# Kernel optimization log

Hardware: AMD Instinct MI355X
Metric: run time of the kernel (lower is better)

The kernel has to match this reference:

```python
import jax, jax.numpy as jnp
import numpy as np

N_NODES = 100000
N_EDGES = 1600000
HIDDEN_DIM = 64
EIGS_DIM = 32


def setup_inputs() -> dict:
    key = jax.random.key(0)
    k1, k2, k3, k4, k5 = jax.random.split(key, 5)
    q = jax.random.normal(k1, (N_NODES, HIDDEN_DIM), dtype=jnp.float32)
    k = jax.random.normal(k2, (N_NODES, HIDDEN_DIM), dtype=jnp.float32)
    v = jax.random.normal(k3, (N_NODES, HIDDEN_DIM), dtype=jnp.float32)
    eigs = jax.random.normal(k4, (N_NODES, EIGS_DIM), dtype=jnp.float32)
    lambda0 = jnp.zeros((1,), dtype=jnp.float32)  # nn.Parameter(torch.zeros(1))
    indices = jax.random.randint(k5, (2, N_EDGES), 0, N_NODES, dtype=jnp.int64)
    return {"q": q, "k": k, "v": v, "eigs": eigs, "lambda0": lambda0,
            "indices": indices}


def reference(q, k, v, eigs, lambda0, indices):
    n = q.shape[0]
    inv_sqrt_dim = 1.0 / jnp.sqrt(jnp.asarray(q.shape[1], dtype=q.dtype))
    i0 = indices[0]  # destination/row node per edge
    i1 = indices[1]  # source/col node per edge

    # per-edge attention logits: gather-dot-product
    x = jnp.sum(q[i0] * k[i1], axis=-1) * inv_sqrt_dim          # [E]
    y = jnp.sum(eigs[i0] * eigs[i1], axis=-1)                   # [E]
    s = x + jnp.exp(lambda0[0]) * y                             # [E]

    # sparse softmax: clamp(exp(s), -5, 5) then segment-normalize by row sum
    e = jnp.clip(jnp.exp(s), -5.0, 5.0)                         # [E]
    denom = jax.ops.segment_sum(e, i0, num_segments=n)          # [N]
    denom = jnp.where(denom == 0.0, 1.0, denom)
    w = e / denom[i0]                                           # [E]

    # spmm: out[r] = sum_{edges with row r} w_e * v[col_e]
    out = jax.ops.segment_sum(w[:, None] * v[i1], i0, num_segments=n)  # [N, D]
    return out
```

## Files before the change

### kernel.cpp

```cpp
#include <hip/hip_runtime.h>
#include <hip/hip_fp16.h>


#define HD 64
#define ED 32
#define CAP 64
#define RPP 256
#define PSHIFT 8
#define D1 15
#define SLICE 16
#define NBIN 512
#define SPILL_CAP 65536

struct h4 { __half2 a, b; };

__global__ void p1_wide_kernel(const int* __restrict__ idx, int n_edges,
                               int NP, int chunk, long long pcap,
                               int* __restrict__ part,
                               long long* __restrict__ spill,
                               int* __restrict__ spill_cnt,
                               int* __restrict__ flag,
                               const float* __restrict__ kf,
                               const float* __restrict__ vf,
                               const float* __restrict__ ef,
                               __half* __restrict__ k16,
                               __half* __restrict__ v16,
                               __half* __restrict__ e16,
                               long long nk4, long long ne4) {
    extern __shared__ int sm[];
    int tid = threadIdx.x;

    if (blockIdx.x >= NBIN) {
        if (k16 == nullptr) return;
        long long gt = (long long)(blockIdx.x - NBIN) * 256 + tid;
        long long gs = (long long)(gridDim.x - NBIN) * 256;
        for (long long t = gt; t < nk4; t += gs) {
            float4 f = ((const float4*)kf)[t];
            h4 h;
            h.a = __floats2half2_rn(f.x, f.y);
            h.b = __floats2half2_rn(f.z, f.w);
            ((h4*)k16)[t] = h;
        }
        for (long long t = gt; t < nk4; t += gs) {
            float4 f = ((const float4*)vf)[t];
            h4 h;
            h.a = __floats2half2_rn(f.x, f.y);
            h.b = __floats2half2_rn(f.z, f.w);
            ((h4*)v16)[t] = h;
        }
        for (long long t = gt; t < ne4; t += gs) {
            float4 f = ((const float4*)ef)[t];
            h4 h;
            h.a = __floats2half2_rn(f.x, f.y);
            h.b = __floats2half2_rn(f.z, f.w);
            ((h4*)e16)[t] = h;
        }
        return;
    }

    int* cnt  = sm;
    int* bins = sm + NP;

    for (int i = tid; i < NP; i += 256) cnt[i] = 0;
    __syncthreads();

    int e0 = blockIdx.x * chunk;
    int n  = n_edges - e0; if (n > chunk) n = chunk; if (n < 0) n = 0;

    for (int i = tid; i < n; i += 256) {
        int e = e0 + i;
        int r = idx[e];
        int c = idx[n_edges + e];
        int p = r >> PSHIFT;
        int w = ((r & (RPP - 1)) << 17) | c;
        int pos = atomicAdd(&cnt[p], 1);
        if (pos < D1) {
            bins[p * D1 + pos] = w;
        } else {
            int s = atomicAdd(spill_cnt, 1);
            if (s < SPILL_CAP) spill[s] = ((long long)r << 32) | (unsigned)c;
            else *flag = 1;
        }
    }
    __syncthreads();

    int g16 = tid >> 4;
    int sl  = tid & 15;
    for (int p = g16; p < NP; p += 16) {
        int m = cnt[p]; if (m > D1) m = D1;
        long long base = (long long)p * pcap + (long long)blockIdx.x * SLICE;
        int val = (sl == 0) ? m
                : (sl <= m) ? bins[p * D1 + sl - 1] : 0;
        part[base + sl] = val;
    }
}

__global__ void p2_bucket_kernel(const int* __restrict__ part,
                                 const long long* __restrict__ spill,
                                 const int* __restrict__ spill_cnt,
                                 const int* __restrict__ flag,
                                 const int* __restrict__ idx, int n_edges,
                                 int* __restrict__ count,
                                 int* __restrict__ bucket, int n_nodes,
                                 long long pcap) {
    __shared__ int cnt2[RPP / 2];
    __shared__ int win[(RPP / 2) * CAP];
    int tid = threadIdx.x;
    if (tid < RPP / 2) cnt2[tid] = 0;
    __syncthreads();

    int p    = blockIdx.x >> 1;
    int half = blockIdx.x & 1;

    if (*flag == 0) {
        int g  = tid >> 4;
        int sl = tid & 15;
        const int* prow = part + (long long)p * pcap;
        for (int b = g; b < NBIN; b += 16) {
            int val = prow[b * SLICE + sl];
            int m = __shfl(val, 0, 16);
            if (m > D1) m = D1;
            if (sl >= 1 && sl <= m) {
                int rl = val >> 17;
                if ((rl >> 7) == half) {
                    int rh = rl & 127;
                    int c  = val & 0x1FFFF;
                    int pos = atomicAdd(&cnt2[rh], 1);
                    if (pos < CAP) win[(rh << 6) + pos] = c;
                }
            }
        }
        int ns = *spill_cnt; if (ns > SPILL_CAP) ns = SPILL_CAP;
        for (int i = tid; i < ns; i += 256) {
            long long wc = spill[i];
            int r = (int)(wc >> 32);
            if ((r >> PSHIFT) == p && (((r >> 7) & 1) == half)) {
                int rh = r & 127;
                int c  = (int)(wc & 0xFFFFFFFFLL);
                int pos = atomicAdd(&cnt2[rh], 1);
                if (pos < CAP) win[(rh << 6) + pos] = c;
            }
        }
    } else {
        for (int i = tid; i < n_edges; i += 256) {
            int r = idx[i];
            if ((r >> PSHIFT) == p && (((r >> 7) & 1) == half)) {
                int rh = r & 127;
                int c  = idx[n_edges + i];
                int pos = atomicAdd(&cnt2[rh], 1);
                if (pos < CAP) win[(rh << 6) + pos] = c;
            }
        }
    }
    __syncthreads();

    int r0 = (p << PSHIFT) + (half << 7);
    int rows = n_nodes - r0;
    if (rows > RPP / 2) rows = RPP / 2;
    if (rows > 0) {
        int nint4 = rows * (CAP / 4);
        int4* dst = (int4*)(bucket + (long long)r0 * CAP);
        const int4* src = (const int4*)win;
        for (int i = tid; i < nint4; i += 256) dst[i] = src[i];
        if (tid < rows) count[r0 + tid] = cnt2[tid];
    }
}

__global__ void bucket_scatter_kernel(const int* __restrict__ idx,
                                      int* __restrict__ count,
                                      int* __restrict__ bucket, int n_edges) {
    int t = blockIdx.x * blockDim.x + threadIdx.x;
    if (t < n_edges) {
        int r = idx[t];
        int c = idx[n_edges + t];
        int p = atomicAdd(&count[r], 1);
        if (p < CAP) bucket[(long long)r * CAP + p] = c;
    }
}

__global__ void row16_kernel(const float* __restrict__ q,
                             const __half* __restrict__ k16,
                             const __half* __restrict__ v16,
                             const float* __restrict__ eigs,
                             const __half* __restrict__ e16,
                             const float* __restrict__ lambda0,
                             const int* __restrict__ counts,
                             const int* __restrict__ col,
                             const float* __restrict__ kf,
                             const float* __restrict__ vf,
                             const int* __restrict__ idx, int n_edges,
                             float* __restrict__ out, int n_nodes) {
    long long tid = (long long)blockIdx.x * blockDim.x + threadIdx.x;
    int r = (int)(tid >> 6);
    if (r >= n_nodes) return;
    int lane = threadIdx.x & 63;
    int sub = lane & 15;
    int grp = lane >> 4;

    int deg = counts[r];
    const float expL = __expf(lambda0[0]);

    if (deg > CAP) {
        float qs = q[(long long)r * HD + lane] * 0.125f;
        float gs = (lane < ED) ? eigs[(long long)r * ED + lane] * expL : 0.f;
        float accs = 0.f, den = 0.f;
        for (int base = 0; base < n_edges; base += 64) {
            int e = base + lane;
            int rr = (e < n_edges) ? idx[e] : -1;
            int cc = (e < n_edges) ? idx[n_edges + e] : 0;
            unsigned long long mm = __ballot(rr == r);
            while (mm) {
                int b = __ffsll(mm) - 1;
                mm &= mm - 1;
                int c = __shfl(cc, b, 64);
                float kb = kf[(long long)c * HD + lane];
                float gb = (lane < ED) ? eigs[(long long)c * ED + lane] : 0.f;
                float s = qs * kb + gs * gb;
                #pragma unroll
                for (int off = 32; off > 0; off >>= 1) s += __shfl_xor(s, off, 64);
                float e1 = fminf(__expf(s), 5.0f);
                den += e1;
                accs += e1 * vf[(long long)c * HD + lane];
            }
        }
        float inv = (den == 0.f) ? 1.f : __frcp_rn(den);
        out[(long long)r * HD + lane] = accs * inv;
        return;
    }

    long long start = (long long)r * CAP;

    float4 qa = *(const float4*)(q    + (long long)r * HD + sub * 4);
    float2 ga = *(const float2*)(eigs + (long long)r * ED + sub * 2);
    qa.x *= 0.125f; qa.y *= 0.125f; qa.z *= 0.125f; qa.w *= 0.125f;
    ga.x *= expL;   ga.y *= expL;

    float4 acc = make_float4(0.f, 0.f, 0.f, 0.f);
    float den = 0.f;

    for (int base = 0; base < deg; base += 64) {
        int m = deg - base; if (m > 64) m = 64;
        int cl = (lane < m) ? col[start + base + lane] : 0;
        for (int j = 0; j < m; j += 16) {
            int c1 = __shfl(cl, j + grp,      64);
            int c2 = __shfl(cl, j + 4 + grp,  64);
            int c3 = __shfl(cl, j + 8 + grp,  64);
            int c4 = __shfl(cl, j + 12 + grp, 64);
            h4 kb1 = *(const h4*)(k16 + (long long)c1 * HD + sub * 4);
            __half2 gh1 = *(const __half2*)(e16 + (long long)c1 * ED + sub * 2);
            h4 vv1 = *(const h4*)(v16 + (long long)c1 * HD + sub * 4);
            h4 kb2 = *(const h4*)(k16 + (long long)c2 * HD + sub * 4);
            __half2 gh2 = *(const __half2*)(e16 + (long long)c2 * ED + sub * 2);
            h4 vv2 = *(const h4*)(v16 + (long long)c2 * HD + sub * 4);
            h4 kb3 = *(const h4*)(k16 + (long long)c3 * HD + sub * 4);
            __half2 gh3 = *(const __half2*)(e16 + (long long)c3 * ED + sub * 2);
            h4 vv3 = *(const h4*)(v16 + (long long)c3 * HD + sub * 4);
            h4 kb4 = *(const h4*)(k16 + (long long)c4 * HD + sub * 4);
            __half2 gh4 = *(const __half2*)(e16 + (long long)c4 * ED + sub * 2);
            h4 vv4 = *(const h4*)(v16 + (long long)c4 * HD + sub * 4);

            float s1 = qa.x*__low2float(kb1.a) + qa.y*__high2float(kb1.a)
                     + qa.z*__low2float(kb1.b) + qa.w*__high2float(kb1.b)
                     + ga.x*__low2float(gh1)   + ga.y*__high2float(gh1);
            float s2 = qa.x*__low2float(kb2.a) + qa.y*__high2float(kb2.a)
                     + qa.z*__low2float(kb2.b) + qa.w*__high2float(kb2.b)
                     + ga.x*__low2float(gh2)   + ga.y*__high2float(gh2);
            float s3 = qa.x*__low2float(kb3.a) + qa.y*__high2float(kb3.a)
                     + qa.z*__low2float(kb3.b) + qa.w*__high2float(kb3.b)
                     + ga.x*__low2float(gh3)   + ga.y*__high2float(gh3);
            float s4 = qa.x*__low2float(kb4.a) + qa.y*__high2float(kb4.a)
                     + qa.z*__low2float(kb4.b) + qa.w*__high2float(kb4.b)
                     + ga.x*__low2float(gh4)   + ga.y*__high2float(gh4);
            #pragma unroll
            for (int off = 8; off > 0; off >>= 1) {
                s1 += __shfl_xor(s1, off, 64);
                s2 += __shfl_xor(s2, off, 64);
                s3 += __shfl_xor(s3, off, 64);
                s4 += __shfl_xor(s4, off, 64);
            }
            float e1 = fminf(__expf(s1), 5.0f);
            float e2 = fminf(__expf(s2), 5.0f);
            float e3 = fminf(__expf(s3), 5.0f);
            float e4 = fminf(__expf(s4), 5.0f);

            if (j + grp < m) {
                den += e1;
                acc.x += e1 * __low2float(vv1.a); acc.y += e1 * __high2float(vv1.a);
                acc.z += e1 * __low2float(vv1.b); acc.w += e1 * __high2float(vv1.b);
            }
            if (j + 4 + grp < m) {
                den += e2;
                acc.x += e2 * __low2float(vv2.a); acc.y += e2 * __high2float(vv2.a);
                acc.z += e2 * __low2float(vv2.b); acc.w += e2 * __high2float(vv2.b);
            }
            if (j + 8 + grp < m) {
                den += e3;
                acc.x += e3 * __low2float(vv3.a); acc.y += e3 * __high2float(vv3.a);
                acc.z += e3 * __low2float(vv3.b); acc.w += e3 * __high2float(vv3.b);
            }
            if (j + 12 + grp < m) {
                den += e4;
                acc.x += e4 * __low2float(vv4.a); acc.y += e4 * __high2float(vv4.a);
                acc.z += e4 * __low2float(vv4.b); acc.w += e4 * __high2float(vv4.b);
            }
        }
    }

    #pragma unroll
    for (int off = 16; off < 64; off <<= 1) {
        acc.x += __shfl_xor(acc.x, off, 64);
        acc.y += __shfl_xor(acc.y, off, 64);
        acc.z += __shfl_xor(acc.z, off, 64);
        acc.w += __shfl_xor(acc.w, off, 64);
        den   += __shfl_xor(den,   off, 64);
    }

    if (grp == 0) {
        float inv = (den == 0.0f) ? 1.0f : __frcp_rn(den);
        float4 o = make_float4(acc.x * inv, acc.y * inv, acc.z * inv, acc.w * inv);
        *(float4*)(out + (long long)r * HD + sub * 4) = o;
    }
}

__global__ void row_kernel(const float* __restrict__ q, const float* __restrict__ k,
                           const float* __restrict__ v, const float* __restrict__ eigs,
                           const float* __restrict__ lambda0,
                           const int* __restrict__ counts,
                           const int* __restrict__ col,
                           const int* __restrict__ idx, int n_edges,
                           float* __restrict__ out, int n_nodes) {
    long long tid = (long long)blockIdx.x * blockDim.x + threadIdx.x;
    int r = (int)(tid >> 6);
    if (r >= n_nodes) return;
    int lane = threadIdx.x & 63;
    int sub = lane & 15;
    int grp = lane >> 4;

    int deg = counts[r];
    const float expL = __expf(lambda0[0]);

    if (deg > CAP) {
        float qs = q[(long long)r * HD + lane] * 0.125f;
        float gs = (lane < ED) ? eigs[(long long)r * ED + lane] * expL : 0.f;
        float accs = 0.f, den = 0.f;
        for (int base = 0; base < n_edges; base += 64) {
            int e = base + lane;
            int rr = (e < n_edges) ? idx[e] : -1;
            int cc = (e < n_edges) ? idx[n_edges + e] : 0;
            unsigned long long mm = __ballot(rr == r);
            while (mm) {
                int b = __ffsll(mm) - 1;
                mm &= mm - 1;
                int c = __shfl(cc, b, 64);
                float kb = k[(long long)c * HD + lane];
                float gb = (lane < ED) ? eigs[(long long)c * ED + lane] : 0.f;
                float s = qs * kb + gs * gb;
                #pragma unroll
                for (int off = 32; off > 0; off >>= 1) s += __shfl_xor(s, off, 64);
                float e1 = fminf(__expf(s), 5.0f);
                den += e1;
                accs += e1 * v[(long long)c * HD + lane];
            }
        }
        float inv = (den == 0.f) ? 1.f : __frcp_rn(den);
        out[(long long)r * HD + lane] = accs * inv;
        return;
    }

    long long start = (long long)r * CAP;

    float4 qa = *(const float4*)(q    + (long long)r * HD + sub * 4);
    float2 ga = *(const float2*)(eigs + (long long)r * ED + sub * 2);
    qa.x *= 0.125f; qa.y *= 0.125f; qa.z *= 0.125f; qa.w *= 0.125f;
    ga.x *= expL;   ga.y *= expL;

    float4 acc = make_float4(0.f, 0.f, 0.f, 0.f);
    float den = 0.f;

    for (int base = 0; base < deg; base += 64) {
        int m = deg - base; if (m > 64) m = 64;
        int cl = (lane < m) ? col[start + base + lane] : 0;
        for (int j = 0; j < m; j += 8) {
            int c1 = __shfl(cl, j + grp,     64);
            int c2 = __shfl(cl, j + 4 + grp, 64);
            float4 kb1 = *(const float4*)(k    + (long long)c1 * HD + sub * 4);
            float2 gb1 = *(const float2*)(eigs + (long long)c1 * ED + sub * 2);
            float4 vv1 = *(const float4*)(v    + (long long)c1 * HD + sub * 4);
            float4 kb2 = *(const float4*)(k    + (long long)c2 * HD + sub * 4);
            float2 gb2 = *(const float2*)(eigs + (long long)c2 * ED + sub * 2);
            float4 vv2 = *(const float4*)(v    + (long long)c2 * HD + sub * 4);

            float s1 = qa.x*kb1.x + qa.y*kb1.y + qa.z*kb1.z + qa.w*kb1.w
                     + ga.x*gb1.x + ga.y*gb1.y;
            float s2 = qa.x*kb2.x + qa.y*kb2.y + qa.z*kb2.z + qa.w*kb2.w
                     + ga.x*gb2.x + ga.y*gb2.y;
            #pragma unroll
            for (int off = 8; off > 0; off >>= 1) {
                s1 += __shfl_xor(s1, off, 64);
                s2 += __shfl_xor(s2, off, 64);
            }
            float e1 = fminf(__expf(s1), 5.0f);
            float e2 = fminf(__expf(s2), 5.0f);

            if (j + grp < m) {
                den += e1;
                acc.x += e1 * vv1.x; acc.y += e1 * vv1.y;
                acc.z += e1 * vv1.z; acc.w += e1 * vv1.w;
            }
            if (j + 4 + grp < m) {
                den += e2;
                acc.x += e2 * vv2.x; acc.y += e2 * vv2.y;
                acc.z += e2 * vv2.z; acc.w += e2 * vv2.w;
            }
        }
    }

    #pragma unroll
    for (int off = 16; off < 64; off <<= 1) {
        acc.x += __shfl_xor(acc.x, off, 64);
        acc.y += __shfl_xor(acc.y, off, 64);
        acc.z += __shfl_xor(acc.z, off, 64);
        acc.w += __shfl_xor(acc.w, off, 64);
        den   += __shfl_xor(den,   off, 64);
    }

    if (grp == 0) {
        float inv = (den == 0.0f) ? 1.0f : __frcp_rn(den);
        float4 o = make_float4(acc.x * inv, acc.y * inv, acc.z * inv, acc.w * inv);
        *(float4*)(out + (long long)r * HD + sub * 4) = o;
    }
}

__global__ void edge_fused_kernel(const float* __restrict__ q,
                                  const float* __restrict__ k,
                                  const float* __restrict__ v,
                                  const float* __restrict__ eigs,
                                  const float* __restrict__ lambda0,
                                  const int* __restrict__ idx,
                                  float* __restrict__ denom,
                                  float* __restrict__ out, int n_edges) {
    long long gid = (long long)blockIdx.x * blockDim.x + threadIdx.x;
    int lane = threadIdx.x & 63;
    int edge = (int)(gid >> 4);
    int sub  = (int)(gid & 15);
    int valid = (edge < n_edges);
    int ec = valid ? edge : (n_edges - 1);
    int i0 = idx[ec];
    int i1 = idx[n_edges + ec];
    const float expL = __expf(lambda0[0]);
    float4 qa = *(const float4*)(q + (long long)i0 * HD + sub * 4);
    float4 kb = *(const float4*)(k + (long long)i1 * HD + sub * 4);
    float c = (qa.x*kb.x + qa.y*kb.y + qa.z*kb.z + qa.w*kb.w) * 0.125f;
    float2 ea = *(const float2*)(eigs + (long long)i0 * ED + sub * 2);
    float2 eb = *(const float2*)(eigs + (long long)i1 * ED + sub * 2);
    c += expL * (ea.x * eb.x + ea.y * eb.y);
    #pragma unroll
    for (int off = 8; off > 0; off >>= 1) c += __shfl_xor(c, off, 64);
    float e = fminf(__expf(c), 5.0f);
    if (valid && sub == 0) atomicAdd(&denom[i0], e);
    #pragma unroll
    for (int j = 0; j < 4; ++j) {
        float ej = __shfl(e,     j * 16, 64);
        int   r  = __shfl(i0,    j * 16, 64);
        int   s  = __shfl(i1,    j * 16, 64);
        int   vj = __shfl(valid, j * 16, 64);
        if (vj) {
            float vv = v[(long long)s * HD + lane];
            atomicAdd(&out[(long long)r * HD + lane], ej * vv);
        }
    }
}

__global__ void normalize_kernel(float* __restrict__ out,
                                 const float* __restrict__ denom, int n_nodes) {
    int t = blockIdx.x * blockDim.x + threadIdx.x;
    int total = n_nodes * (HD / 4);
    if (t >= total) return;
    int row = t >> 4;
    float d = denom[row];
    float inv = (d == 0.0f) ? 1.0f : __frcp_rn(d);
    float4* o4 = (float4*)out;
    float4 x = o4[t];
    x.x *= inv; x.y *= inv; x.z *= inv; x.w *= inv;
    o4[t] = x;
}

extern "C" void kernel_launch(void* const* d_in, const int* in_sizes, int n_in,
                              void* d_out, int out_size, void* d_ws, size_t ws_size,
                              hipStream_t stream) {
    const float* q       = (const float*)d_in[0];
    const float* k       = (const float*)d_in[1];
    const float* v       = (const float*)d_in[2];
    const float* eigs    = (const float*)d_in[3];
    const float* lambda0 = (const float*)d_in[4];
    const int*   idx     = (const int*)d_in[5];

    const int n_edges = in_sizes[5] / 2;
    const int n_nodes = in_sizes[0] / HD;

    const int NP = (n_nodes + RPP - 1) / RPP;
    const int eb = (n_edges + 255) / 256;
    long long rthreads = (long long)n_nodes * 64;
    const int rb = (int)((rthreads + 255) / 256);

    size_t smbytes = (size_t)NP * (1 + D1) * sizeof(int);
    bool geom_ok = (smbytes <= 60 * 1024) && (n_nodes <= 0x1FFFF);

    size_t sp  = 8 + (size_t)SPILL_CAP * sizeof(long long);
    size_t h16 = (size_t)n_nodes * (HD + HD + ED) * sizeof(__half);
    size_t fixed = (size_t)n_nodes * sizeof(int)
                 + (size_t)n_nodes * CAP * sizeof(int);
    size_t pbytes = (size_t)NP * (size_t)NBIN * SLICE * sizeof(int);
    size_t n16 = h16 + fixed + pbytes + sp;
    size_t n32 = fixed + pbytes + sp;
    size_t need2 = fixed;

    long long pcap = (long long)NBIN * SLICE;
    int chunk = (n_edges + NBIN - 1) / NBIN;

    if (geom_ok && ws_size >= n16) {
        char* base = (char*)d_ws;
        __half* k16 = (__half*)base;
        __half* v16 = k16 + (size_t)n_nodes * HD;
        __half* e16 = v16 + (size_t)n_nodes * HD;
        int* count  = (int*)(e16 + (size_t)n_nodes * ED);
        int* bucket = count + n_nodes;
        int* part   = bucket + (size_t)n_nodes * CAP;
        int* spill_cnt = part + (size_t)NP * pcap;
        int* flag      = spill_cnt + 1;
        size_t soff = (size_t)((char*)(flag + 1) - base);
        soff = (soff + 7) & ~(size_t)7;
        long long* spill = (long long*)(base + soff);

        hipMemsetAsync(spill_cnt, 0, 2 * sizeof(int), stream);

        p1_wide_kernel<<<2 * NBIN, 256, smbytes, stream>>>(
            idx, n_edges, NP, chunk, pcap, part, spill, spill_cnt, flag,
            k, v, eigs, k16, v16, e16,
            (long long)n_nodes * HD / 4, (long long)n_nodes * ED / 4);
        p2_bucket_kernel<<<2 * NP, 256, 0, stream>>>(
            part, spill, spill_cnt, flag, idx, n_edges, count, bucket,
            n_nodes, pcap);
        row16_kernel<<<rb, 256, 0, stream>>>(q, k16, v16, eigs, e16, lambda0,
                                             count, bucket, k, v, idx, n_edges,
                                             (float*)d_out, n_nodes);
    } else if (geom_ok && ws_size >= n32) {
        char* base = (char*)d_ws;
        int* count  = (int*)base;
        int* bucket = count + n_nodes;
        int* part   = bucket + (size_t)n_nodes * CAP;
        int* spill_cnt = part + (size_t)NP * pcap;
        int* flag      = spill_cnt + 1;
        size_t soff = (size_t)((char*)(flag + 1) - base);
        soff = (soff + 7) & ~(size_t)7;
        long long* spill = (long long*)(base + soff);

        hipMemsetAsync(spill_cnt, 0, 2 * sizeof(int), stream);

        p1_wide_kernel<<<2 * NBIN, 256, smbytes, stream>>>(
            idx, n_edges, NP, chunk, pcap, part, spill, spill_cnt, flag,
            nullptr, nullptr, nullptr, nullptr, nullptr, nullptr, 0, 0);
        p2_bucket_kernel<<<2 * NP, 256, 0, stream>>>(
            part, spill, spill_cnt, flag, idx, n_edges, count, bucket,
            n_nodes, pcap);
        row_kernel<<<rb, 256, 0, stream>>>(q, k, v, eigs, lambda0, count, bucket,
                                           idx, n_edges, (float*)d_out, n_nodes);
    } else if (ws_size >= need2) {
        int* count  = (int*)d_ws;
        int* bucket = count + n_nodes;
        hipMemsetAsync(count, 0, (size_t)n_nodes * sizeof(int), stream);
        bucket_scatter_kernel<<<eb, 256, 0, stream>>>(idx, count, bucket, n_edges);
        row_kernel<<<rb, 256, 0, stream>>>(q, k, v, eigs, lambda0, count, bucket,
                                           idx, n_edges, (float*)d_out, n_nodes);
    } else {
        float* denom = (float*)d_ws;
        hipMemsetAsync(denom, 0, (size_t)n_nodes * sizeof(float), stream);
        hipMemsetAsync(d_out, 0, (size_t)out_size * sizeof(float), stream);
        long long threads = (long long)n_edges * 16;
        int grid = (int)((threads + 255) / 256);
        edge_fused_kernel<<<grid, 256, 0, stream>>>(q, k, v, eigs, lambda0, idx,
                                                    denom, (float*)d_out, n_edges);
        int n4 = n_nodes * (HD / 4);
        normalize_kernel<<<(n4 + 255) / 256, 256, 0, stream>>>((float*)d_out,
                                                               denom, n_nodes);
    }
}
```

Measured before the change: 261.1 us.

## Dynamically distribute fp16 conversion via atomic tile counter; split row kernel launch

The k/v/eigs fp16 conversion used to run only in dedicated blocks with a static grid-stride split. It now runs as a work-stealing loop: every block, including binning blocks once they finish, grabs 4096-element tiles from a global atomic counter, so conversion work spreads over all blocks. The row kernel is also launched as two half-range launches instead of one. This adds one atomic and two block barriers per tile, plus an extra kernel launch.

Result: slower. 279.8 us (+7.1%).

```diff
diff --git a/kernel.cpp b/kernel.cpp
--- a/kernel.cpp
+++ b/kernel.cpp
@@ -11,6 +11,7 @@
 #define SLICE 16
 #define NBIN 512
 #define SPILL_CAP 65536
+#define CVT_TILE 4096
 
 struct h4 { __half2 a, b; };
 
@@ -20,78 +21,91 @@
                                long long* __restrict__ spill,
                                int* __restrict__ spill_cnt,
                                int* __restrict__ flag,
+                               int* __restrict__ cvt_tick,
                                const float* __restrict__ kf,
                                const float* __restrict__ vf,
                                const float* __restrict__ ef,
                                __half* __restrict__ k16,
                                __half* __restrict__ v16,
                                __half* __restrict__ e16,
-                               long long nk4, long long ne4) {
+                               long long nk4, long long ne4, int ntiles) {
     extern __shared__ int sm[];
+    __shared__ int tk;
     int tid = threadIdx.x;
 
-    if (blockIdx.x >= NBIN) {
-        if (k16 == nullptr) return;
-        long long gt = (long long)(blockIdx.x - NBIN) * 256 + tid;
-        long long gs = (long long)(gridDim.x - NBIN) * 256;
-        for (long long t = gt; t < nk4; t += gs) {
-            float4 f = ((const float4*)kf)[t];
+    if (blockIdx.x < NBIN) {
+        int* cnt  = sm;
+        int* bins = sm + NP;
+
+        for (int i = tid; i < NP; i += 256) cnt[i] = 0;
+        __syncthreads();
+
+        int e0 = blockIdx.x * chunk;
+        int n  = n_edges - e0; if (n > chunk) n = chunk; if (n < 0) n = 0;
+
+        for (int i = tid; i < n; i += 256) {
+            int e = e0 + i;
+            int r = idx[e];
+            int c = idx[n_edges + e];
+            int p = r >> PSHIFT;
+            int w = ((r & (RPP - 1)) << 17) | c;
+            int pos = atomicAdd(&cnt[p], 1);
+            if (pos < D1) {
+                bins[p * D1 + pos] = w;
+            } else {
+                int s = atomicAdd(spill_cnt, 1);
+                if (s < SPILL_CAP) spill[s] = ((long long)r << 32) | (unsigned)c;
+                else *flag = 1;
+            }
+        }
+        __syncthreads();
+
+        int g16 = tid >> 4;
+        int sl  = tid & 15;
+        for (int p = g16; p < NP; p += 16) {
+            int m = cnt[p]; if (m > D1) m = D1;
+            long long base = (long long)p * pcap
+                           + (long long)blockIdx.x * SLICE;
+            int val = (sl == 0) ? m
+                    : (sl <= m) ? bins[p * D1 + sl - 1] : 0;
+            part[base + sl] = val;
+        }
+        __syncthreads();
+    }
+
+    if (k16 == nullptr) return;
+    for (;;) {
+        if (tid == 0) tk = atomicAdd(cvt_tick, 1);
+        __syncthreads();
+        int t = tk;
+        __syncthreads();
+        if (t >= ntiles) break;
+        long long u0 = (long long)t * CVT_TILE;
+        long long total = 2 * nk4 + ne4;
+        for (int i = tid; i < CVT_TILE; i += 256) {
+            long long u = u0 + i;
+            if (u >= total) break;
+            float4 f;
             h4 h;
-            h.a = __floats2half2_rn(f.x, f.y);
-            h.b = __floats2half2_rn(f.z, f.w);
-            ((h4*)k16)[t] = h;
-        }
-        for (long long t = gt; t < nk4; t += gs) {
-            float4 f = ((const float4*)vf)[t];
-            h4 h;
-            h.a = __floats2half2_rn(f.x, f.y);
-            h.b = __floats2half2_rn(f.z, f.w);
-            ((h4*)v16)[t] = h;
-        }
-        for (long long t = gt; t < ne4; t += gs) {
-            float4 f = ((const float4*)ef)[t];
-            h4 h;
-            h.a = __floats2half2_rn(f.x, f.y);
-            h.b = __floats2half2_rn(f.z, f.w);
-            ((h4*)e16)[t] = h;
-        }
-        return;
-    }
-
-    int* cnt  = sm;
-    int* bins = sm + NP;
-
-    for (int i = tid; i < NP; i += 256) cnt[i] = 0;
-    __syncthreads();
-
-    int e0 = blockIdx.x * chunk;
-    int n  = n_edges - e0; if (n > chunk) n = chunk; if (n < 0) n = 0;
-
-    for (int i = tid; i < n; i += 256) {
-        int e = e0 + i;
-        int r = idx[e];
-        int c = idx[n_edges + e];
-        int p = r >> PSHIFT;
-        int w = ((r & (RPP - 1)) << 17) | c;
-        int pos = atomicAdd(&cnt[p], 1);
-        if (pos < D1) {
-            bins[p * D1 + pos] = w;
-        } else {
-            int s = atomicAdd(spill_cnt, 1);
-            if (s < SPILL_CAP) spill[s] = ((long long)r << 32) | (unsigned)c;
-            else *flag = 1;
-        }
-    }
-    __syncthreads();
-
-    int g16 = tid >> 4;
-    int sl  = tid & 15;
-    for (int p = g16; p < NP; p += 16) {
-        int m = cnt[p]; if (m > D1) m = D1;
-        long long base = (long long)p * pcap + (long long)blockIdx.x * SLICE;
-        int val = (sl == 0) ? m
-                : (sl <= m) ? bins[p * D1 + sl - 1] : 0;
-        part[base + sl] = val;
+            if (u < nk4) {
+                f = ((const float4*)kf)[u];
+                h.a = __floats2half2_rn(f.x, f.y);
+                h.b = __floats2half2_rn(f.z, f.w);
+                ((h4*)k16)[u] = h;
+            } else if (u < 2 * nk4) {
+                long long w = u - nk4;
+                f = ((const float4*)vf)[w];
+                h.a = __floats2half2_rn(f.x, f.y);
+                h.b = __floats2half2_rn(f.z, f.w);
+                ((h4*)v16)[w] = h;
+            } else {
+                long long w = u - 2 * nk4;
+                f = ((const float4*)ef)[w];
+                h.a = __floats2half2_rn(f.x, f.y);
+                h.b = __floats2half2_rn(f.z, f.w);
+                ((h4*)e16)[w] = h;
+            }
+        }
     }
 }
 
@@ -189,10 +203,10 @@
                              const float* __restrict__ kf,
                              const float* __restrict__ vf,
                              const int* __restrict__ idx, int n_edges,
-                             float* __restrict__ out, int n_nodes) {
+                             float* __restrict__ out, int row0, int row1) {
     long long tid = (long long)blockIdx.x * blockDim.x + threadIdx.x;
-    int r = (int)(tid >> 6);
-    if (r >= n_nodes) return;
+    int r = row0 + (int)(tid >> 6);
+    if (r >= row1) return;
     int lane = threadIdx.x & 63;
     int sub = lane & 15;
     int grp = lane >> 4;
@@ -506,7 +520,7 @@
     size_t smbytes = (size_t)NP * (1 + D1) * sizeof(int);
     bool geom_ok = (smbytes <= 60 * 1024) && (n_nodes <= 0x1FFFF);
 
-    size_t sp  = 8 + (size_t)SPILL_CAP * sizeof(long long);
+    size_t sp  = 16 + (size_t)SPILL_CAP * sizeof(long long);
     size_t h16 = (size_t)n_nodes * (HD + HD + ED) * sizeof(__half);
     size_t fixed = (size_t)n_nodes * sizeof(int)
                  + (size_t)n_nodes * CAP * sizeof(int);
@@ -528,22 +542,32 @@
         int* part   = bucket + (size_t)n_nodes * CAP;
         int* spill_cnt = part + (size_t)NP * pcap;
         int* flag      = spill_cnt + 1;
-        size_t soff = (size_t)((char*)(flag + 1) - base);
+        int* cvt_tick  = spill_cnt + 2;
+        size_t soff = (size_t)((char*)(spill_cnt + 4) - base);
         soff = (soff + 7) & ~(size_t)7;
         long long* spill = (long long*)(base + soff);
 
-        hipMemsetAsync(spill_cnt, 0, 2 * sizeof(int), stream);
+        hipMemsetAsync(spill_cnt, 0, 4 * sizeof(int), stream);
+
+        long long nk4 = (long long)n_nodes * HD / 4;
+        long long ne4 = (long long)n_nodes * ED / 4;
+        int ntiles = (int)((2 * nk4 + ne4 + CVT_TILE - 1) / CVT_TILE);
 
         p1_wide_kernel<<<2 * NBIN, 256, smbytes, stream>>>(
             idx, n_edges, NP, chunk, pcap, part, spill, spill_cnt, flag,
-            k, v, eigs, k16, v16, e16,
-            (long long)n_nodes * HD / 4, (long long)n_nodes * ED / 4);
+            cvt_tick, k, v, eigs, k16, v16, e16, nk4, ne4, ntiles);
         p2_bucket_kernel<<<2 * NP, 256, 0, stream>>>(
             part, spill, spill_cnt, flag, idx, n_edges, count, bucket,
             n_nodes, pcap);
-        row16_kernel<<<rb, 256, 0, stream>>>(q, k16, v16, eigs, e16, lambda0,
-                                             count, bucket, k, v, idx, n_edges,
-                                             (float*)d_out, n_nodes);
+        int rh = (n_nodes + 1) / 2;
+        int rb1 = (int)(((long long)rh * 64 + 255) / 256);
+        int rb2 = (int)(((long long)(n_nodes - rh) * 64 + 255) / 256);
+        row16_kernel<<<rb1, 256, 0, stream>>>(q, k16, v16, eigs, e16, lambda0,
+                                              count, bucket, k, v, idx, n_edges,
+                                              (float*)d_out, 0, rh);
+        row16_kernel<<<rb2, 256, 0, stream>>>(q, k16, v16, eigs, e16, lambda0,
+                                              count, bucket, k, v, idx, n_edges,
+                                              (float*)d_out, rh, n_nodes);
     } else if (geom_ok && ws_size >= n32) {
         char* base = (char*)d_ws;
         int* count  = (int*)base;
@@ -551,15 +575,17 @@
         int* part   = bucket + (size_t)n_nodes * CAP;
         int* spill_cnt = part + (size_t)NP * pcap;
         int* flag      = spill_cnt + 1;
-        size_t soff = (size_t)((char*)(flag + 1) - base);
+        int* cvt_tick  = spill_cnt + 2;
+        size_t soff = (size_t)((char*)(spill_cnt + 4) - base);
         soff = (soff + 7) & ~(size_t)7;
         long long* spill = (long long*)(base + soff);
 
-        hipMemsetAsync(spill_cnt, 0, 2 * sizeof(int), stream);
+        hipMemsetAsync(spill_cnt, 0, 4 * sizeof(int), stream);
 
         p1_wide_kernel<<<2 * NBIN, 256, smbytes, stream>>>(
             idx, n_edges, NP, chunk, pcap, part, spill, spill_cnt, flag,
-            nullptr, nullptr, nullptr, nullptr, nullptr, nullptr, 0, 0);
+            cvt_tick, nullptr, nullptr, nullptr, nullptr, nullptr, nullptr,
+            0, 0, 0);
         p2_bucket_kernel<<<2 * NP, 256, 0, stream>>>(
             part, spill, spill_cnt, flag, idx, n_edges, count, bucket,
             n_nodes, pcap);
```

## Use per-block spill buffers and unroll edge binning and fp16 conversion loops

Applied to the files above, without the earlier changes.

Replaces the single global spill counter and buffer with one spill region and header per binning block. Overflowing edges now use a shared-memory atomic instead of a global one, and the memset that reset the global counter is removed. The edge binning loop and the fp32-to-fp16 conversion loops are unrolled by four so more loads are in flight. In exchange, each bucket block must now scan all 512 spill headers, and any per-block overflow forces the slow fallback path that scans every edge.

After: 244.6 us. 1.07x faster.

```diff
diff --git a/kernel.cpp b/kernel.cpp
--- a/kernel.cpp
+++ b/kernel.cpp
@@ -10,7 +10,7 @@
 #define D1 15
 #define SLICE 16
 #define NBIN 512
-#define SPILL_CAP 65536
+#define SPCAP_B 512
 
 struct h4 { __half2 a, b; };
 
@@ -18,8 +18,7 @@
                                int NP, int chunk, long long pcap,
                                int* __restrict__ part,
                                long long* __restrict__ spill,
-                               int* __restrict__ spill_cnt,
-                               int* __restrict__ flag,
+                               int* __restrict__ sphdr,
                                const float* __restrict__ kf,
                                const float* __restrict__ vf,
                                const float* __restrict__ ef,
@@ -28,31 +27,78 @@
                                __half* __restrict__ e16,
                                long long nk4, long long ne4) {
     extern __shared__ int sm[];
+    __shared__ int spn;
     int tid = threadIdx.x;
 
     if (blockIdx.x >= NBIN) {
         if (k16 == nullptr) return;
         long long gt = (long long)(blockIdx.x - NBIN) * 256 + tid;
-        long long gs = (long long)(gridDim.x - NBIN) * 256;
-        for (long long t = gt; t < nk4; t += gs) {
+        long long gs = (long long)NBIN * 256;
+        long long t;
+        t = gt;
+        for (; t + 3 * gs < nk4; t += 4 * gs) {
+            float4 f0 = ((const float4*)kf)[t];
+            float4 f1 = ((const float4*)kf)[t + gs];
+            float4 f2 = ((const float4*)kf)[t + 2 * gs];
+            float4 f3 = ((const float4*)kf)[t + 3 * gs];
+            h4 h0, h1, h2, h3;
+            h0.a = __floats2half2_rn(f0.x, f0.y); h0.b = __floats2half2_rn(f0.z, f0.w);
+            h1.a = __floats2half2_rn(f1.x, f1.y); h1.b = __floats2half2_rn(f1.z, f1.w);
+            h2.a = __floats2half2_rn(f2.x, f2.y); h2.b = __floats2half2_rn(f2.z, f2.w);
+            h3.a = __floats2half2_rn(f3.x, f3.y); h3.b = __floats2half2_rn(f3.z, f3.w);
+            ((h4*)k16)[t] = h0;
+            ((h4*)k16)[t + gs] = h1;
+            ((h4*)k16)[t + 2 * gs] = h2;
+            ((h4*)k16)[t + 3 * gs] = h3;
+        }
+        for (; t < nk4; t += gs) {
             float4 f = ((const float4*)kf)[t];
             h4 h;
-            h.a = __floats2half2_rn(f.x, f.y);
-            h.b = __floats2half2_rn(f.z, f.w);
+            h.a = __floats2half2_rn(f.x, f.y); h.b = __floats2half2_rn(f.z, f.w);
             ((h4*)k16)[t] = h;
         }
-        for (long long t = gt; t < nk4; t += gs) {
+        t = gt;
+        for (; t + 3 * gs < nk4; t += 4 * gs) {
+            float4 f0 = ((const float4*)vf)[t];
+            float4 f1 = ((const float4*)vf)[t + gs];
+            float4 f2 = ((const float4*)vf)[t + 2 * gs];
+            float4 f3 = ((const float4*)vf)[t + 3 * gs];
+            h4 h0, h1, h2, h3;
+            h0.a = __floats2half2_rn(f0.x, f0.y); h0.b = __floats2half2_rn(f0.z, f0.w);
+            h1.a = __floats2half2_rn(f1.x, f1.y); h1.b = __floats2half2_rn(f1.z, f1.w);
+            h2.a = __floats2half2_rn(f2.x, f2.y); h2.b = __floats2half2_rn(f2.z, f2.w);
+            h3.a = __floats2half2_rn(f3.x, f3.y); h3.b = __floats2half2_rn(f3.z, f3.w);
+            ((h4*)v16)[t] = h0;
+            ((h4*)v16)[t + gs] = h1;
+            ((h4*)v16)[t + 2 * gs] = h2;
+            ((h4*)v16)[t + 3 * gs] = h3;
+        }
+        for (; t < nk4; t += gs) {
             float4 f = ((const float4*)vf)[t];
             h4 h;
-            h.a = __floats2half2_rn(f.x, f.y);
-            h.b = __floats2half2_rn(f.z, f.w);
+            h.a = __floats2half2_rn(f.x, f.y); h.b = __floats2half2_rn(f.z, f.w);
             ((h4*)v16)[t] = h;
         }
-        for (long long t = gt; t < ne4; t += gs) {
+        t = gt;
+        for (; t + 3 * gs < ne4; t += 4 * gs) {
+            float4 f0 = ((const float4*)ef)[t];
+            float4 f1 = ((const float4*)ef)[t + gs];
+            float4 f2 = ((const float4*)ef)[t + 2 * gs];
+            float4 f3 = ((const float4*)ef)[t + 3 * gs];
+            h4 h0, h1, h2, h3;
+            h0.a = __floats2half2_rn(f0.x, f0.y); h0.b = __floats2half2_rn(f0.z, f0.w);
+            h1.a = __floats2half2_rn(f1.x, f1.y); h1.b = __floats2half2_rn(f1.z, f1.w);
+            h2.a = __floats2half2_rn(f2.x, f2.y); h2.b = __floats2half2_rn(f2.z, f2.w);
+            h3.a = __floats2half2_rn(f3.x, f3.y); h3.b = __floats2half2_rn(f3.z, f3.w);
+            ((h4*)e16)[t] = h0;
+            ((h4*)e16)[t + gs] = h1;
+            ((h4*)e16)[t + 2 * gs] = h2;
+            ((h4*)e16)[t + 3 * gs] = h3;
+        }
+        for (; t < ne4; t += gs) {
             float4 f = ((const float4*)ef)[t];
             h4 h;
-            h.a = __floats2half2_rn(f.x, f.y);
-            h.b = __floats2half2_rn(f.z, f.w);
+            h.a = __floats2half2_rn(f.x, f.y); h.b = __floats2half2_rn(f.z, f.w);
             ((h4*)e16)[t] = h;
         }
         return;
@@ -60,14 +106,42 @@
 
     int* cnt  = sm;
     int* bins = sm + NP;
-
+    long long* myspill = spill + (long long)blockIdx.x * SPCAP_B;
+
+    if (tid == 0) spn = 0;
     for (int i = tid; i < NP; i += 256) cnt[i] = 0;
     __syncthreads();
 
     int e0 = blockIdx.x * chunk;
     int n  = n_edges - e0; if (n > chunk) n = chunk; if (n < 0) n = 0;
 
-    for (int i = tid; i < n; i += 256) {
+    int i = tid;
+    for (; i + 768 < n; i += 1024) {
+        int e  = e0 + i;
+        int r0 = idx[e];
+        int r1 = idx[e + 256];
+        int r2 = idx[e + 512];
+        int r3 = idx[e + 768];
+        int c0 = idx[n_edges + e];
+        int c1 = idx[n_edges + e + 256];
+        int c2 = idx[n_edges + e + 512];
+        int c3 = idx[n_edges + e + 768];
+        #pragma unroll
+        for (int u = 0; u < 4; ++u) {
+            int r = (u == 0) ? r0 : (u == 1) ? r1 : (u == 2) ? r2 : r3;
+            int c = (u == 0) ? c0 : (u == 1) ? c1 : (u == 2) ? c2 : c3;
+            int p = r >> PSHIFT;
+            int w = ((r & (RPP - 1)) << 17) | c;
+            int pos = atomicAdd(&cnt[p], 1);
+            if (pos < D1) {
+                bins[p * D1 + pos] = w;
+            } else {
+                int s = atomicAdd(&spn, 1);
+                if (s < SPCAP_B) myspill[s] = ((long long)r << 32) | (unsigned)c;
+            }
+        }
+    }
+    for (; i < n; i += 256) {
         int e = e0 + i;
         int r = idx[e];
         int c = idx[n_edges + e];
@@ -77,12 +151,13 @@
         if (pos < D1) {
             bins[p * D1 + pos] = w;
         } else {
-            int s = atomicAdd(spill_cnt, 1);
-            if (s < SPILL_CAP) spill[s] = ((long long)r << 32) | (unsigned)c;
-            else *flag = 1;
+            int s = atomicAdd(&spn, 1);
+            if (s < SPCAP_B) myspill[s] = ((long long)r << 32) | (unsigned)c;
         }
     }
     __syncthreads();
+
+    if (tid == 0) sphdr[blockIdx.x] = (spn > SPCAP_B) ? -1 : spn;
 
     int g16 = tid >> 4;
     int sl  = tid & 15;
@@ -97,22 +172,27 @@
 
 __global__ void p2_bucket_kernel(const int* __restrict__ part,
                                  const long long* __restrict__ spill,
-                                 const int* __restrict__ spill_cnt,
-                                 const int* __restrict__ flag,
+                                 const int* __restrict__ sphdr,
                                  const int* __restrict__ idx, int n_edges,
                                  int* __restrict__ count,
                                  int* __restrict__ bucket, int n_nodes,
                                  long long pcap) {
     __shared__ int cnt2[RPP / 2];
     __shared__ int win[(RPP / 2) * CAP];
+    __shared__ int cata;
     int tid = threadIdx.x;
+    if (tid == 0) cata = 0;
     if (tid < RPP / 2) cnt2[tid] = 0;
     __syncthreads();
 
+    for (int b = tid; b < NBIN; b += 256)
+        if (sphdr[b] < 0) cata = 1;
+    __syncthreads();
+
     int p    = blockIdx.x >> 1;
     int half = blockIdx.x & 1;
 
-    if (*flag == 0) {
+    if (cata == 0) {
         int g  = tid >> 4;
         int sl = tid & 15;
         const int* prow = part + (long long)p * pcap;
@@ -130,15 +210,18 @@
                 }
             }
         }
-        int ns = *spill_cnt; if (ns > SPILL_CAP) ns = SPILL_CAP;
-        for (int i = tid; i < ns; i += 256) {
-            long long wc = spill[i];
-            int r = (int)(wc >> 32);
-            if ((r >> PSHIFT) == p && (((r >> 7) & 1) == half)) {
-                int rh = r & 127;
-                int c  = (int)(wc & 0xFFFFFFFFLL);
-                int pos = atomicAdd(&cnt2[rh], 1);
-                if (pos < CAP) win[(rh << 6) + pos] = c;
+        for (int b = tid; b < NBIN; b += 256) {
+            int ns = sphdr[b];
+            const long long* sp = spill + (long long)b * SPCAP_B;
+            for (int i2 = 0; i2 < ns; ++i2) {
+                long long wc = sp[i2];
+                int r = (int)(wc >> 32);
+                if ((r >> PSHIFT) == p && (((r >> 7) & 1) == half)) {
+                    int rh = r & 127;
+                    int c  = (int)(wc & 0xFFFFFFFFLL);
+                    int pos = atomicAdd(&cnt2[rh], 1);
+                    if (pos < CAP) win[(rh << 6) + pos] = c;
+                }
             }
         }
     } else {
@@ -506,13 +589,14 @@
     size_t smbytes = (size_t)NP * (1 + D1) * sizeof(int);
     bool geom_ok = (smbytes <= 60 * 1024) && (n_nodes <= 0x1FFFF);
 
-    size_t sp  = 8 + (size_t)SPILL_CAP * sizeof(long long);
     size_t h16 = (size_t)n_nodes * (HD + HD + ED) * sizeof(__half);
     size_t fixed = (size_t)n_nodes * sizeof(int)
                  + (size_t)n_nodes * CAP * sizeof(int);
     size_t pbytes = (size_t)NP * (size_t)NBIN * SLICE * sizeof(int);
-    size_t n16 = h16 + fixed + pbytes + sp;
-    size_t n32 = fixed + pbytes + sp;
+    size_t hdrb = (size_t)NBIN * sizeof(int);
+    size_t spb  = (size_t)NBIN * SPCAP_B * sizeof(long long);
+    size_t n16 = h16 + fixed + pbytes + hdrb + spb + 16;
+    size_t n32 = fixed + pbytes + hdrb + spb + 16;
     size_t need2 = fixed;
 
     long long pcap = (long long)NBIN * SLICE;
@@ -526,21 +610,17 @@
         int* count  = (int*)(e16 + (size_t)n_nodes * ED);
         int* bucket = count + n_nodes;
         int* part   = bucket + (size_t)n_nodes * CAP;
-        int* spill_cnt = part + (size_t)NP * pcap;
-        int* flag      = spill_cnt + 1;
-        size_t soff = (size_t)((char*)(flag + 1) - base);
+        int* sphdr  = part + (size_t)NP * pcap;
+        size_t soff = (size_t)((char*)(sphdr + NBIN) - base);
         soff = (soff + 7) & ~(size_t)7;
         long long* spill = (long long*)(base + soff);
 
-        hipMemsetAsync(spill_cnt, 0, 2 * sizeof(int), stream);
-
         p1_wide_kernel<<<2 * NBIN, 256, smbytes, stream>>>(
-            idx, n_edges, NP, chunk, pcap, part, spill, spill_cnt, flag,
+            idx, n_edges, NP, chunk, pcap, part, spill, sphdr,
             k, v, eigs, k16, v16, e16,
             (long long)n_nodes * HD / 4, (long long)n_nodes * ED / 4);
         p2_bucket_kernel<<<2 * NP, 256, 0, stream>>>(
-            part, spill, spill_cnt, flag, idx, n_edges, count, bucket,
-            n_nodes, pcap);
+            part, spill, sphdr, idx, n_edges, count, bucket, n_nodes, pcap);
         row16_kernel<<<rb, 256, 0, stream>>>(q, k16, v16, eigs, e16, lambda0,
                                              count, bucket, k, v, idx, n_edges,
                                              (float*)d_out, n_nodes);
@@ -549,20 +629,16 @@
         int* count  = (int*)base;
         int* bucket = count + n_nodes;
         int* part   = bucket + (size_t)n_nodes * CAP;
-        int* spill_cnt = part + (size_t)NP * pcap;
-        int* flag      = spill_cnt + 1;
-        size_t soff = (size_t)((char*)(flag + 1) - base);
+        int* sphdr  = part + (size_t)NP * pcap;
+        size_t soff = (size_t)((char*)(sphdr + NBIN) - base);
         soff = (soff + 7) & ~(size_t)7;
         long long* spill = (long long*)(base + soff);
 
-        hipMemsetAsync(spill_cnt, 0, 2 * sizeof(int), stream);
-
         p1_wide_kernel<<<2 * NBIN, 256, smbytes, stream>>>(
-            idx, n_edges, NP, chunk, pcap, part, spill, spill_cnt, flag,
+            idx, n_edges, NP, chunk, pcap, part, spill, sphdr,
             nullptr, nullptr, nullptr, nullptr, nullptr, nullptr, 0, 0);
         p2_bucket_kernel<<<2 * NP, 256, 0, stream>>>(
-            part, spill, spill_cnt, flag, idx, n_edges, count, bucket,
-            n_nodes, pcap);
+            part, spill, sphdr, idx, n_edges, count, bucket, n_nodes, pcap);
         row_kernel<<<rb, 256, 0, stream>>>(q, k, v, eigs, lambda0, count, bucket,
                                            idx, n_edges, (float*)d_out, n_nodes);
     } else if (ws_size >= need2) {
```
